# Optimization experiments

Hardware: AMD Instinct MI355X
Metric: run time of the kernel (lower is better)

Reference implementation:

```python
import jax, jax.numpy as jnp
import numpy as np

B, D_IN, H, D_OUT = 2048, 1024, 2048, 1024
MAX_STEPS = 12
EPS = 0.01


def setup_inputs() -> dict:
    key = jax.random.key(0)
    ks = jax.random.split(key, 8)
    s_in = 1.0 / np.sqrt(D_IN + H)
    s_h = 1.0 / np.sqrt(H)
    return {
        "x": jax.random.normal(ks[0], (B, D_IN), jnp.float32),
        "h": jax.random.normal(ks[1], (B, H), jnp.float32),
        "W_hidden": jax.random.normal(ks[2], (H, D_IN + H), jnp.float32) * s_in,
        "b_hidden": jnp.zeros((H,), jnp.float32),
        "w_halt": jax.random.normal(ks[3], (H,), jnp.float32) * s_h,
        "b_halt": jnp.float32(-2.0),  # bias low so several ponder steps are taken
        "W_out": jax.random.normal(ks[4], (D_OUT, H), jnp.float32) * s_h,
        "b_out": jnp.zeros((D_OUT,), jnp.float32),
    }


def reference(x, h, W_hidden, b_hidden, w_halt, b_halt, W_out, b_out):
    # Batched ACT halting loop, unrolled to MAX_STEPS via lax.scan.
    def step(s, t):
        # step 0 of the original uses x+1 as a "first step" flag
        xin = jnp.where(t == 0, x + 1.0, x)          # [B, D_IN]
        z = jnp.concatenate([xin, s], axis=-1)        # [B, D_IN+H]
        s_new = z @ W_hidden.T + b_hidden             # [B, H]
        p = jax.nn.sigmoid(s_new @ w_halt + b_halt)   # [B]
        out = s_new @ W_out.T + b_out                 # [B, D_OUT]
        return s_new, (s_new, p, out)

    _, (states, probs, outs) = jax.lax.scan(step, h, jnp.arange(MAX_STEPS))
    # states: [T,B,H], probs: [T,B], outs: [T,B,D_OUT]

    cum = jnp.cumsum(probs, axis=0)                   # [T,B]
    reached = cum >= (1.0 - EPS)
    # first step where cumulative halt prob crosses the threshold (cap at T-1)
    n = jnp.where(jnp.any(reached, axis=0), jnp.argmax(reached, axis=0), MAX_STEPS - 1)  # [B]

    t_idx = jnp.arange(MAX_STEPS)[:, None]            # [T,1]
    before = t_idx < n[None, :]                       # [T,B]
    R = 1.0 - jnp.sum(jnp.where(before, probs, 0.0), axis=0)  # [B] remainder
    w = jnp.where(before, probs, jnp.where(t_idx == n[None, :], R[None, :], 0.0))  # [T,B]

    output = jnp.einsum("tb,tbd->bd", w, outs)        # [B, D_OUT]
    hidden = jnp.einsum("tb,tbh->bh", w, states)      # [B, H]
    ponder = (n + 1).astype(jnp.float32) + R          # [B]
    return output, hidden, ponder
```

## Files before the change

### kernel.cpp

```cpp
#include <hip/hip_runtime.h>
#include <hip/hip_bf16.h>
#include <cstdint>

#define B_SZ   2048
#define D_INN  1024
#define H_SZ   2048
#define D_OUTN 1024
#define TMAX   12
#define LDW    3072
#define NSL    12
#define SLC    256

typedef _Float16 f16;
typedef __attribute__((ext_vector_type(8))) _Float16 f16x8;
typedef __attribute__((ext_vector_type(4))) float    f32x4;

typedef const __attribute__((address_space(1))) uint32_t* gptr_t;
typedef __attribute__((address_space(3))) uint32_t*       lptr_t;
__device__ inline void gld16(const void* g, void* l) {
    __builtin_amdgcn_global_load_lds((gptr_t)g, (lptr_t)l, 16, 0, 0);
}

template<int BN>
__global__ __launch_bounds__(512, 4) void gemm16(
    const f16* __restrict__ A, int lda,
    const f16* __restrict__ Bm, int ldb,
    const float* __restrict__ Cadd,
    const f16*  __restrict__ Cadd16,
    const float* __restrict__ radd,
    float* __restrict__ Cf,
    f16* __restrict__ Cs,
    float* __restrict__ hid,
    const float* __restrict__ wvec,
    int hacc,
    f16* __restrict__ hid16,
    int ldc, int K, int nx)
{
    constexpr int WN = BN / 64;
    constexpr int NV = (BN == 128) ? 3 : 2;
    __shared__ __align__(16) f16 As[3][64 * 64];
    __shared__ __align__(16) f16 Bs[3][BN * 64];
    const int tid  = threadIdx.x;
    const int wave = tid >> 6;
    const int lane = tid & 63;

    const int nwg = gridDim.x;
    const int cpx = nwg >> 3;
    const int bid = (blockIdx.x & 7) * cpx + (blockIdx.x >> 3);
    const int m0 = (bid / nx) * 64, n0 = (bid % nx) * BN;

    const int wr = wave >> 2, wc = wave & 3;
    const int fr = lane & 15, fq = lane >> 4;

    const int acs = tid ^ ((tid >> 3) & 7);
    const f16* gA = A + (size_t)(m0 + (acs >> 3)) * lda + (acs & 7) * 8;
    const int adst = wave << 9;
    const int bcs1 = tid ^ ((tid >> 3) & 7);
    const f16* gB1 = Bm + (size_t)(n0 + (bcs1 >> 3)) * ldb + (bcs1 & 7) * 8;
    const int bdst1 = wave << 9;
    const f16* gB2 = nullptr;
    int bdst2 = 0;
    if constexpr (BN == 128) {
        const int bc2 = tid + 512;
        const int bcs2 = bc2 ^ ((bc2 >> 3) & 7);
        gB2 = Bm + (size_t)(n0 + (bcs2 >> 3)) * ldb + (bcs2 & 7) * 8;
        bdst2 = 4096 + (wave << 9);
    }

    int offA[2][2], offB[WN][2];
#pragma unroll
    for (int m = 0; m < 2; ++m)
#pragma unroll
        for (int ks = 0; ks < 2; ++ks) {
            const int row = wr * 32 + m * 16 + fr;
            offA[m][ks] = row * 64 + (((ks * 4 + fq) ^ (row & 7)) << 3);
        }
#pragma unroll
    for (int n = 0; n < WN; ++n)
#pragma unroll
        for (int ks = 0; ks < 2; ++ks) {
            const int row = wc * (WN * 16) + n * 16 + fr;
            offB[n][ks] = row * 64 + (((ks * 4 + fq) ^ (row & 7)) << 3);
        }

    auto STAGE = [&](int buf, int ko) {
        gld16(gA + ko,  &As[buf][0] + adst);
        gld16(gB1 + ko, &Bs[buf][0] + bdst1);
        if constexpr (BN == 128) gld16(gB2 + ko, &Bs[buf][0] + bdst2);
    };

    f32x4 acc[2][WN] = {};

    STAGE(0, 0);
    const int nk = K >> 6;
    int cur = 0;
    for (int ki = 0; ki < nk; ++ki) {
        const int nxt = (cur == 2) ? 0 : cur + 1;
        if (ki + 1 < nk) {
            STAGE(nxt, (ki + 1) << 6);
            asm volatile("s_waitcnt vmcnt(%0)" :: "i"(NV) : "memory");
        } else {
            asm volatile("s_waitcnt vmcnt(0)" ::: "memory");
        }
        __builtin_amdgcn_s_barrier();
        asm volatile("" ::: "memory");

        f16x8 a[2][2], b[WN][2];
#pragma unroll
        for (int m = 0; m < 2; ++m)
#pragma unroll
            for (int ks = 0; ks < 2; ++ks)
                a[m][ks] = *(const f16x8*)(&As[cur][offA[m][ks]]);
#pragma unroll
        for (int n = 0; n < WN; ++n)
#pragma unroll
            for (int ks = 0; ks < 2; ++ks)
                b[n][ks] = *(const f16x8*)(&Bs[cur][offB[n][ks]]);
#pragma unroll
        for (int ks = 0; ks < 2; ++ks)
#pragma unroll
            for (int m = 0; m < 2; ++m)
#pragma unroll
                for (int n = 0; n < WN; ++n)
                    acc[m][n] = __builtin_amdgcn_mfma_f32_16x16x32_f16(
                        a[m][ks], b[n][ks], acc[m][n], 0, 0, 0);
        cur = nxt;
    }

    float wr8[2][4];
    if (hid) {
#pragma unroll
        for (int m = 0; m < 2; ++m)
#pragma unroll
            for (int r = 0; r < 4; ++r)
                wr8[m][r] = wvec[m0 + wr * 32 + m * 16 + fq * 4 + r];
    }
#pragma unroll
    for (int m = 0; m < 2; ++m) {
#pragma unroll
        for (int n = 0; n < WN; ++n) {
#pragma unroll
            for (int r = 0; r < 4; ++r) {
                const int row = m0 + wr * 32 + m * 16 + fq * 4 + r;
                const int col = n0 + wc * (WN * 16) + n * 16 + fr;
                const size_t o = (size_t)row * ldc + col;
                float v = acc[m][n][r];
                if (Cadd)   v += Cadd[o];
                if (Cadd16) v += (float)Cadd16[o];
                if (radd)   v += radd[col];
                if (Cf) Cf[o] = v;
                if (Cs) Cs[o] = (f16)v;
                if (hid) {
                    const float w = wr8[m][r];
                    if (!hacc) {
                        const float hv = w * v;
                        hid[o] = hv;
                        if (hid16) hid16[o] = (f16)hv;
                    } else if (w != 0.f) {
                        const float hv = hid[o] + w * v;
                        hid[o] = hv;
                        if (hid16) hid16[o] = (f16)hv;
                    } else if (hid16) {
                        hid16[o] = (f16)hid[o];
                    }
                }
            }
        }
    }
}

__global__ __launch_bounds__(256) void cast16(
    const float* __restrict__ src, int ld, int cols,
    f16* __restrict__ dst, int total8)
{
    const int i = blockIdx.x * 256 + threadIdx.x;
    if (i >= total8) return;
    const int idx = i * 8;
    const int r = idx / cols, c = idx % cols;
    const float4 v0 = *(const float4*)(src + (size_t)r * ld + c);
    const float4 v1 = *(const float4*)(src + (size_t)r * ld + c + 4);
    f16x8 o;
    o[0]=(f16)v0.x; o[1]=(f16)v0.y; o[2]=(f16)v0.z; o[3]=(f16)v0.w;
    o[4]=(f16)v1.x; o[5]=(f16)v1.y; o[6]=(f16)v1.z; o[7]=(f16)v1.w;
    *(f16x8*)(dst + idx) = o;
}

__global__ __launch_bounds__(256) void rowsum_kernel(
    const float* __restrict__ W, int ld, int K, float* __restrict__ out)
{
    const int j = blockIdx.x;
    const int tid = threadIdx.x;
    float s = 0.f;
    for (int k = tid; k < K; k += 256) s += W[(size_t)j * ld + k];
#pragma unroll
    for (int off = 32; off; off >>= 1) s += __shfl_down(s, off);
    __shared__ float red[4];
    if ((tid & 63) == 0) red[tid >> 6] = s;
    __syncthreads();
    if (tid == 0) out[j] = red[0] + red[1] + red[2] + red[3];
}

__global__ __launch_bounds__(256) void transpose_w(
    const float* __restrict__ in, float* __restrict__ out, int R, int C)
{
    __shared__ float t[32][33];
    const int bc = blockIdx.x * 32, br = blockIdx.y * 32;
    const int tx = threadIdx.x & 31, ty = threadIdx.x >> 5;
#pragma unroll
    for (int i = 0; i < 32; i += 8)
        t[ty + i][tx] = in[(size_t)(br + ty + i) * C + bc + tx];
    __syncthreads();
#pragma unroll
    for (int i = 0; i < 32; i += 8)
        out[(size_t)(bc + ty + i) * R + br + tx] = t[tx][ty + i];
}

__global__ __launch_bounds__(256) void init_u0(
    const float* __restrict__ w, double* __restrict__ u)
{
    const int i = blockIdx.x * 256 + threadIdx.x;
    if (i < H_SZ) u[i] = (double)w[i];
}

__global__ __launch_bounds__(256) void gemv_t(
    const float* __restrict__ WT, const double* __restrict__ uin,
    double* __restrict__ uout)
{
    const int i = blockIdx.x;
    const int tid = threadIdx.x;
    const float* row = WT + (size_t)(D_INN + i) * H_SZ;
    double acc = 0.0;
    for (int j = tid; j < H_SZ; j += 256) acc += (double)row[j] * uin[j];
#pragma unroll
    for (int off = 32; off; off >>= 1) acc += __shfl_down(acc, off);
    __shared__ double red[4];
    if ((tid & 63) == 0) red[tid >> 6] = acc;
    __syncthreads();
    if (tid == 0) uout[i] = red[0] + red[1] + red[2] + red[3];
}

__global__ __launch_bounds__(256) void batch_wx(
    const float* __restrict__ WT, const double* __restrict__ U,
    double* __restrict__ XU, double* __restrict__ XS)
{
    const int k = blockIdx.x;
    const int tid = threadIdx.x;
    const float* row = WT + (size_t)k * H_SZ;
    double au[TMAX] = {}, av[TMAX] = {};
    for (int j = tid; j < H_SZ; j += 256) {
        const double w = (double)row[j];
        double pref = 0.0;
#pragma unroll
        for (int t = 0; t < TMAX; ++t) {
            const double u = U[(size_t)t * H_SZ + j];
            pref += u;
            au[t] += w * u;
            av[t] += w * pref;
        }
    }
    __shared__ double red[4][2 * TMAX];
#pragma unroll
    for (int t = 0; t < TMAX; ++t) {
#pragma unroll
        for (int off = 32; off; off >>= 1) {
            au[t] += __shfl_down(au[t], off);
            av[t] += __shfl_down(av[t], off);
        }
    }
    if ((tid & 63) == 0) {
#pragma unroll
        for (int t = 0; t < TMAX; ++t) {
            red[tid >> 6][t] = au[t];
            red[tid >> 6][TMAX + t] = av[t];
        }
    }
    __syncthreads();
    if (tid == 0) {
#pragma unroll
        for (int t = 0; t < TMAX; ++t) {
            XS[(size_t)t * D_INN + k] = red[0][t] + red[1][t] + red[2][t] + red[3][t];
            XU[(size_t)t * D_INN + k] = red[0][TMAX+t] + red[1][TMAX+t]
                                      + red[2][TMAX+t] + red[3][TMAX+t];
        }
    }
}

__global__ __launch_bounds__(256) void e_kernel(
    const double* __restrict__ XS, const double* __restrict__ U,
    const float* __restrict__ bh, double* __restrict__ E)
{
    const int t = blockIdx.x;
    const int tid = threadIdx.x;
    double a = 0.0;
    for (int k = tid; k < D_INN; k += 256) a += XS[(size_t)t * D_INN + k];
    for (int j = tid; j < H_SZ; j += 256) {
        double v = 0.0;
        for (int s = 0; s <= t; ++s) v += U[(size_t)s * H_SZ + j];
        a += v * (double)bh[j];
    }
#pragma unroll
    for (int off = 32; off; off >>= 1) a += __shfl_down(a, off);
    __shared__ double red[4];
    if ((tid & 63) == 0) red[tid >> 6] = a;
    __syncthreads();
    if (tid == 0) E[t] = red[0] + red[1] + red[2] + red[3];
}

__global__ __launch_bounds__(256) void d_part(
    const float* __restrict__ h, const float* __restrict__ x,
    const double* __restrict__ U, const double* __restrict__ XU,
    double* __restrict__ part)
{
    __shared__ double Us[TMAX][SLC];
    const int blk = blockIdx.x;
    const int sl  = blk % NSL;
    const int br  = (blk / NSL) * 32;
    const int tid = threadIdx.x;
    const int col0 = sl * SLC;
    const bool isH = col0 < H_SZ;
#pragma unroll
    for (int t = 0; t < TMAX; ++t)
        Us[t][tid] = isH ? U[(size_t)(t + 1) * H_SZ + col0 + tid]
                         : XU[(size_t)t * D_INN + (col0 - H_SZ) + tid];
    __syncthreads();
    const int lane8 = tid & 7;
    const int row   = tid >> 3;
    const float* src = isH ? (h + (size_t)(br + row) * H_SZ + col0)
                           : (x + (size_t)(br + row) * D_INN + (col0 - H_SZ));
    double acc[TMAX] = {};
    const int c0 = lane8 * 32;
    for (int c = c0; c < c0 + 32; ++c) {
        const double v = (double)src[c];
#pragma unroll
        for (int t = 0; t < TMAX; ++t) acc[t] += v * Us[t][c];
    }
#pragma unroll
    for (int t = 0; t < TMAX; ++t) {
        acc[t] += __shfl_xor(acc[t], 1, 64);
        acc[t] += __shfl_xor(acc[t], 2, 64);
        acc[t] += __shfl_xor(acc[t], 4, 64);
    }
    if (lane8 == 0) {
#pragma unroll
        for (int t = 0; t < TMAX; ++t)
            part[((size_t)(br + row) * NSL + sl) * TMAX + t] = acc[t];
    }
}

__global__ __launch_bounds__(256) void sched_kernel(
    const double* __restrict__ part, const double* __restrict__ E,
    const float* __restrict__ b_halt,
    float* __restrict__ Wmat, float* __restrict__ ponder)
{
    const int b = blockIdx.x * 256 + threadIdx.x;
    if (b >= B_SZ) return;
    const float bh = b_halt[0];
    float cum = 0.f, R = 0.f;
    int n = -1;
    float w[TMAX];
#pragma unroll
    for (int t = 0; t < TMAX; ++t) {
        double dd = E[t];
#pragma unroll
        for (int sl = 0; sl < NSL; ++sl)
            dd += part[((size_t)b * NSL + sl) * TMAX + t];
        const float p = 1.f / (1.f + expf(-((float)dd + bh)));
        if (n < 0) {
            const float c = cum + p;
            if (c >= 0.99f || t == TMAX - 1) { n = t; R = 1.f - cum; w[t] = R; }
            else { w[t] = p; cum = c; }
        } else {
            w[t] = 0.f;
        }
    }
    ponder[b] = (float)(n + 1) + R;
#pragma unroll
    for (int t = 0; t < TMAX; ++t) Wmat[(size_t)t * B_SZ + b] = w[t];
}

extern "C" void kernel_launch(void* const* d_in, const int* in_sizes, int n_in,
                              void* d_out, int out_size, void* d_ws, size_t ws_size,
                              hipStream_t stream)
{
    const float* x        = (const float*)d_in[0];
    const float* h        = (const float*)d_in[1];
    const float* W_hidden = (const float*)d_in[2];
    const float* b_hidden = (const float*)d_in[3];
    const float* w_halt   = (const float*)d_in[4];
    const float* b_halt   = (const float*)d_in[5];
    const float* W_out    = (const float*)d_in[6];
    const float* b_out    = (const float*)d_in[7];

    float* out    = (float*)d_out;
    float* output = out;
    float* hidden = out + (size_t)B_SZ * D_OUTN;
    float* ponder = hidden + (size_t)B_SZ * H_SZ;

    double* U    = (double*)d_ws;
    double* XU   = U  + (size_t)(TMAX + 1) * H_SZ;
    double* XS   = XU + (size_t)TMAX * D_INN;
    double* E    = XS + (size_t)TMAX * D_INN;
    double* part = E + 16;
    float* rsum  = (float*)(part + (size_t)B_SZ * NSL * TMAX);
    float* Wmat  = rsum + H_SZ;
    float* WT    = Wmat + (size_t)TMAX * B_SZ;
    f16* xh   = (f16*)(WT + (size_t)LDW * H_SZ);
    f16* Wxh  = xh  + (size_t)B_SZ * D_INN;
    f16* sh0  = Wxh + (size_t)H_SZ * D_INN;
    f16* sh1  = sh0 + (size_t)B_SZ * H_SZ;
    f16* Wsh  = sh1 + (size_t)B_SZ * H_SZ;
    f16* Woh  = Wsh + (size_t)H_SZ * H_SZ;
    f16* xc16 = Woh + (size_t)D_OUTN * H_SZ;
    f16* hid16 = xh;

    const dim3 blk(256);
    const dim3 gblk(512);

    cast16<<<dim3(B_SZ * D_INN / 8 / 256), blk, 0, stream>>>(
        x, D_INN, D_INN, xh, B_SZ * D_INN / 8);
    cast16<<<dim3(B_SZ * H_SZ / 8 / 256), blk, 0, stream>>>(
        h, H_SZ, H_SZ, sh0, B_SZ * H_SZ / 8);
    cast16<<<dim3(H_SZ * D_INN / 8 / 256), blk, 0, stream>>>(
        W_hidden, LDW, D_INN, Wxh, H_SZ * D_INN / 8);
    cast16<<<dim3(H_SZ * H_SZ / 8 / 256), blk, 0, stream>>>(
        W_hidden + D_INN, LDW, H_SZ, Wsh, H_SZ * H_SZ / 8);
    cast16<<<dim3(D_OUTN * H_SZ / 8 / 256), blk, 0, stream>>>(
        W_out, H_SZ, H_SZ, Woh, D_OUTN * H_SZ / 8);

    rowsum_kernel<<<dim3(H_SZ), blk, 0, stream>>>(W_hidden, LDW, D_INN, rsum);

    transpose_w<<<dim3(LDW / 32, H_SZ / 32), blk, 0, stream>>>(
        W_hidden, WT, H_SZ, LDW);
    init_u0<<<dim3(H_SZ / 256), blk, 0, stream>>>(w_halt, U);
    for (int k = 0; k < TMAX; ++k)
        gemv_t<<<dim3(H_SZ), blk, 0, stream>>>(WT, U + (size_t)k * H_SZ,
                                               U + (size_t)(k + 1) * H_SZ);
    batch_wx<<<dim3(D_INN), blk, 0, stream>>>(WT, U, XU, XS);
    e_kernel<<<dim3(TMAX), blk, 0, stream>>>(XS, U, b_hidden, E);
    d_part<<<dim3((B_SZ / 32) * NSL), blk, 0, stream>>>(h, x, U, XU, part);
    sched_kernel<<<dim3(B_SZ / 256), blk, 0, stream>>>(part, E, b_halt,
                                                       Wmat, ponder);

    gemm16<128><<<dim3((B_SZ / 64) * (H_SZ / 128)), gblk, 0, stream>>>(
        xh, D_INN, Wxh, D_INN, nullptr, nullptr, b_hidden, nullptr, xc16,
        nullptr, nullptr, 0, nullptr, H_SZ, D_INN, H_SZ / 128);

    for (int t = 0; t < TMAX; ++t) {
        const f16* ph = (t & 1) ? sh1 : sh0;
        f16*       nh = (t & 1) ? sh0 : sh1;
        gemm16<128><<<dim3((B_SZ / 64) * (H_SZ / 128)), gblk, 0, stream>>>(
            ph, H_SZ, Wsh, H_SZ, nullptr, xc16, (t == 0) ? rsum : nullptr,
            nullptr, nh, hidden, Wmat + (size_t)t * B_SZ, (t > 0),
            (t == TMAX - 1) ? hid16 : nullptr, H_SZ, H_SZ, H_SZ / 128);
    }

    gemm16<64><<<dim3((B_SZ / 64) * (D_OUTN / 64)), gblk, 0, stream>>>(
        hid16, H_SZ, Woh, H_SZ, nullptr, nullptr, b_out, output, nullptr,
        nullptr, nullptr, 0, nullptr, D_OUTN, H_SZ, D_OUTN / 64);
}
```

Baseline: 619.2 us.

## Move hidden-state accumulation out of GEMM epilogue into batched three-step kernel

Removes the per-step read-modify-write of the fp32 hidden accumulator from the recurrent GEMM epilogue. The fp16 states of three consecutive steps go into a triple buffer, and a separate elementwise kernel folds them into hidden once every three steps, skipping rows whose weights are all zero. This cuts fp32 hidden traffic and lightens the GEMM epilogue, but adds four extra kernel launches. It also accumulates from fp16 states rather than the fp32 GEMM values, which costs some precision.

```diff
diff --git a/kernel.cpp b/kernel.cpp
--- a/kernel.cpp
+++ b/kernel.cpp
@@ -25,15 +25,10 @@
 __global__ __launch_bounds__(512, 4) void gemm16(
     const f16* __restrict__ A, int lda,
     const f16* __restrict__ Bm, int ldb,
-    const float* __restrict__ Cadd,
     const f16*  __restrict__ Cadd16,
     const float* __restrict__ radd,
     float* __restrict__ Cf,
     f16* __restrict__ Cs,
-    float* __restrict__ hid,
-    const float* __restrict__ wvec,
-    int hacc,
-    f16* __restrict__ hid16,
     int ldc, int K, int nx)
 {
     constexpr int WN = BN / 64;
@@ -127,14 +122,6 @@
         cur = nxt;
     }
 
-    float wr8[2][4];
-    if (hid) {
-#pragma unroll
-        for (int m = 0; m < 2; ++m)
-#pragma unroll
-            for (int r = 0; r < 4; ++r)
-                wr8[m][r] = wvec[m0 + wr * 32 + m * 16 + fq * 4 + r];
-    }
 #pragma unroll
     for (int m = 0; m < 2; ++m) {
 #pragma unroll
@@ -145,27 +132,62 @@
                 const int col = n0 + wc * (WN * 16) + n * 16 + fr;
                 const size_t o = (size_t)row * ldc + col;
                 float v = acc[m][n][r];
-                if (Cadd)   v += Cadd[o];
                 if (Cadd16) v += (float)Cadd16[o];
                 if (radd)   v += radd[col];
                 if (Cf) Cf[o] = v;
                 if (Cs) Cs[o] = (f16)v;
-                if (hid) {
-                    const float w = wr8[m][r];
-                    if (!hacc) {
-                        const float hv = w * v;
-                        hid[o] = hv;
-                        if (hid16) hid16[o] = (f16)hv;
-                    } else if (w != 0.f) {
-                        const float hv = hid[o] + w * v;
-                        hid[o] = hv;
-                        if (hid16) hid16[o] = (f16)hv;
-                    } else if (hid16) {
-                        hid16[o] = (f16)hid[o];
-                    }
-                }
             }
         }
+    }
+}
+
+__global__ __launch_bounds__(256) void hidacc(
+    const f16* __restrict__ s0, const f16* __restrict__ s1,
+    const f16* __restrict__ s2, const float* __restrict__ Wmat,
+    int tbase, float* __restrict__ hidden, f16* __restrict__ hid16)
+{
+    const int b = blockIdx.x;
+    const float w0 = Wmat[(size_t)(tbase + 0) * B_SZ + b];
+    const float w1 = Wmat[(size_t)(tbase + 1) * B_SZ + b];
+    const float w2 = Wmat[(size_t)(tbase + 2) * B_SZ + b];
+    const bool first = (tbase == 0);
+    const bool last  = (tbase == TMAX - 3);
+    if (!last && w0 == 0.f && w1 == 0.f && w2 == 0.f) return;
+
+    const int tid = threadIdx.x;
+    const size_t o = (size_t)b * H_SZ + tid * 8;
+    float hv[8];
+    if (first) {
+#pragma unroll
+        for (int j = 0; j < 8; ++j) hv[j] = 0.f;
+    } else {
+        const float4 h0 = *(const float4*)(hidden + o);
+        const float4 h1 = *(const float4*)(hidden + o + 4);
+        hv[0]=h0.x; hv[1]=h0.y; hv[2]=h0.z; hv[3]=h0.w;
+        hv[4]=h1.x; hv[5]=h1.y; hv[6]=h1.z; hv[7]=h1.w;
+    }
+    if (w0 != 0.f) {
+        const f16x8 v = *(const f16x8*)(s0 + o);
+#pragma unroll
+        for (int j = 0; j < 8; ++j) hv[j] += w0 * (float)v[j];
+    }
+    if (w1 != 0.f) {
+        const f16x8 v = *(const f16x8*)(s1 + o);
+#pragma unroll
+        for (int j = 0; j < 8; ++j) hv[j] += w1 * (float)v[j];
+    }
+    if (w2 != 0.f) {
+        const f16x8 v = *(const f16x8*)(s2 + o);
+#pragma unroll
+        for (int j = 0; j < 8; ++j) hv[j] += w2 * (float)v[j];
+    }
+    *(float4*)(hidden + o)     = make_float4(hv[0], hv[1], hv[2], hv[3]);
+    *(float4*)(hidden + o + 4) = make_float4(hv[4], hv[5], hv[6], hv[7]);
+    if (last) {
+        f16x8 hh;
+#pragma unroll
+        for (int j = 0; j < 8; ++j) hh[j] = (f16)hv[j];
+        *(f16x8*)(hid16 + o) = hh;
     }
 }
 
@@ -404,14 +426,16 @@
     float* rsum  = (float*)(part + (size_t)B_SZ * NSL * TMAX);
     float* Wmat  = rsum + H_SZ;
     float* WT    = Wmat + (size_t)TMAX * B_SZ;
+    f16* xc16  = (f16*)WT;
+    f16* S2    = (f16*)(WT + (size_t)2 * 1024 * 1024);
+    f16* hid16 = (f16*)(WT + (size_t)4 * 1024 * 1024);
     f16* xh   = (f16*)(WT + (size_t)LDW * H_SZ);
     f16* Wxh  = xh  + (size_t)B_SZ * D_INN;
-    f16* sh0  = Wxh + (size_t)H_SZ * D_INN;
-    f16* sh1  = sh0 + (size_t)B_SZ * H_SZ;
-    f16* Wsh  = sh1 + (size_t)B_SZ * H_SZ;
+    f16* S0   = xh;
+    f16* h16  = Wxh + (size_t)H_SZ * D_INN;
+    f16* S1   = h16 + (size_t)B_SZ * H_SZ;
+    f16* Wsh  = S1  + (size_t)B_SZ * H_SZ;
     f16* Woh  = Wsh + (size_t)H_SZ * H_SZ;
-    f16* xc16 = Woh + (size_t)D_OUTN * H_SZ;
-    f16* hid16 = xh;
 
     const dim3 blk(256);
     const dim3 gblk(512);
@@ -419,7 +443,7 @@
     cast16<<<dim3(B_SZ * D_INN / 8 / 256), blk, 0, stream>>>(
         x, D_INN, D_INN, xh, B_SZ * D_INN / 8);
     cast16<<<dim3(B_SZ * H_SZ / 8 / 256), blk, 0, stream>>>(
-        h, H_SZ, H_SZ, sh0, B_SZ * H_SZ / 8);
+        h, H_SZ, H_SZ, h16, B_SZ * H_SZ / 8);
     cast16<<<dim3(H_SZ * D_INN / 8 / 256), blk, 0, stream>>>(
         W_hidden, LDW, D_INN, Wxh, H_SZ * D_INN / 8);
     cast16<<<dim3(H_SZ * H_SZ / 8 / 256), blk, 0, stream>>>(
@@ -442,19 +466,23 @@
                                                        Wmat, ponder);
 
     gemm16<128><<<dim3((B_SZ / 64) * (H_SZ / 128)), gblk, 0, stream>>>(
-        xh, D_INN, Wxh, D_INN, nullptr, nullptr, b_hidden, nullptr, xc16,
-        nullptr, nullptr, 0, nullptr, H_SZ, D_INN, H_SZ / 128);
-
+        xh, D_INN, Wxh, D_INN, nullptr, b_hidden, nullptr, xc16,
+        H_SZ, D_INN, H_SZ / 128);
+
+    f16* Sb[3] = {S0, S1, S2};
+    const f16* prev = h16;
     for (int t = 0; t < TMAX; ++t) {
-        const f16* ph = (t & 1) ? sh1 : sh0;
-        f16*       nh = (t & 1) ? sh0 : sh1;
+        f16* curS = Sb[t % 3];
         gemm16<128><<<dim3((B_SZ / 64) * (H_SZ / 128)), gblk, 0, stream>>>(
-            ph, H_SZ, Wsh, H_SZ, nullptr, xc16, (t == 0) ? rsum : nullptr,
-            nullptr, nh, hidden, Wmat + (size_t)t * B_SZ, (t > 0),
-            (t == TMAX - 1) ? hid16 : nullptr, H_SZ, H_SZ, H_SZ / 128);
+            prev, H_SZ, Wsh, H_SZ, xc16, (t == 0) ? rsum : nullptr,
+            nullptr, curS, H_SZ, H_SZ, H_SZ / 128);
+        prev = curS;
+        if ((t % 3) == 2)
+            hidacc<<<dim3(B_SZ), blk, 0, stream>>>(
+                S0, S1, S2, Wmat, t - 2, hidden, hid16);
     }
 
     gemm16<64><<<dim3((B_SZ / 64) * (D_OUTN / 64)), gblk, 0, stream>>>(
-        hid16, H_SZ, Woh, H_SZ, nullptr, nullptr, b_out, output, nullptr,
-        nullptr, nullptr, 0, nullptr, D_OUTN, H_SZ, D_OUTN / 64);
-}
+        hid16, H_SZ, Woh, H_SZ, nullptr, b_out, output, nullptr,
+        D_OUTN, H_SZ, D_OUTN / 64);
+}
```

Measured after the change: 577.6 us. 6.7% less time.
